# Optimization experiments

Hardware: AMD Instinct MI355X
Metric: run time of the kernel (lower is better)

The kernel has to match this reference:

```python
import jax, jax.numpy as jnp
import numpy as np

B, S, D_IN, D_OUT = 4, 2048, 2048, 2048
E, R = 8, 8
SCALING = 16.0 / 8.0  # lora_alpha / r
# Dropout (p=0.05) treated as identity (eval mode) for a deterministic reference.

def setup_inputs() -> dict:
    key = jax.random.key(0)
    ks = jax.random.split(key, 8)
    x = jax.random.normal(ks[0], (B, S, D_IN), dtype=jnp.float32)
    base_W = jax.random.normal(ks[1], (D_OUT, D_IN), dtype=jnp.float32) * 0.02
    base_b = jax.random.normal(ks[2], (D_OUT,), dtype=jnp.float32) * 0.02
    shared_A = jax.random.normal(ks[3], (R, D_IN), dtype=jnp.float32) * 0.01
    shared_B = jax.random.normal(ks[4], (D_OUT, R), dtype=jnp.float32) * 0.01
    expert_A = jax.random.normal(ks[5], (E, R, D_IN), dtype=jnp.float32) * 0.01
    expert_B = jax.random.normal(ks[6], (E, D_OUT, R), dtype=jnp.float32) * 0.01
    task_emb = jax.random.normal(ks[7], (E, D_IN), dtype=jnp.float32) * 0.01
    collab_w = jnp.array(0.5, dtype=jnp.float32)
    return {"x": x, "base_W": base_W, "base_b": base_b,
            "shared_A": shared_A, "shared_B": shared_B,
            "expert_A": expert_A, "expert_B": expert_B,
            "task_emb": task_emb, "collab_w": collab_w}

def reference(x, base_W, base_b, shared_A, shared_B, expert_A, expert_B, task_emb, collab_w):
    # base linear: [B,S,D_out]
    base_out = jnp.einsum('bsi,oi->bso', x, base_W) + base_b
    # shared LoRA path
    shared_out = jnp.einsum('bsr,or->bso', jnp.einsum('bsi,ri->bsr', x, shared_A), shared_B) * SCALING
    # soft routing over task experts (task_id=None branch)
    x_mean = x.mean(axis=1)                               # [B,D_in]
    routing = jax.nn.softmax(x_mean @ task_emb.T, axis=-1)  # [B,E]
    t = jnp.einsum('bsi,eri->bser', x, expert_A)          # [B,S,E,R] low-rank
    task_out = jnp.einsum('bser,eor,be->bso', t, expert_B, routing) * SCALING
    cw = jax.nn.sigmoid(collab_w)
    return base_out + cw * shared_out + (1.0 - cw) * task_out
```

## Files before the change

kernel.cpp:

```cpp
#include <hip/hip_runtime.h>
#include <hip/hip_bf16.h>
#include <math.h>

#define BATCH 4
#define SEQ   2048
#define DIN   2048
#define DOUT  2048
#define NEXP  8
#define RANK  8
#define MTOT  (BATCH * SEQ)
#define KE    64
#define KAB   96

typedef __bf16 bf16x8 __attribute__((ext_vector_type(8)));
typedef __bf16 bf16x4 __attribute__((ext_vector_type(4)));
typedef float  f32x4  __attribute__((ext_vector_type(4)));

#define GLOBAL_AS __attribute__((address_space(1)))
#define LDS_AS    __attribute__((address_space(3)))

__global__ __launch_bounds__(256) void prep_all(
    const float* __restrict__ x, const float* __restrict__ W,
    const float* __restrict__ expert_A, const float* __restrict__ shared_A,
    const float* __restrict__ expert_B, const float* __restrict__ shared_B,
    const float* __restrict__ task_emb, const float* __restrict__ collab,
    __bf16* __restrict__ xb, __bf16* __restrict__ Wb,
    __bf16* __restrict__ caug, __bf16* __restrict__ Ab)
{
    const int bid = blockIdx.x;
    const int t = threadIdx.x;
    if (bid < 2048) {
        size_t base = (size_t)bid * 8192 + (size_t)t * 32;
        #pragma unroll
        for (int j = 0; j < 4; ++j) {
            float4 v0 = *(const float4*)&x[base + j * 8];
            float4 v1 = *(const float4*)&x[base + j * 8 + 4];
            bf16x8 h = { (__bf16)v0.x, (__bf16)v0.y, (__bf16)v0.z, (__bf16)v0.w,
                         (__bf16)v1.x, (__bf16)v1.y, (__bf16)v1.z, (__bf16)v1.w };
            *(bf16x8*)&xb[base + j * 8] = h;
        }
    } else if (bid < 6144) {
        size_t idx = (size_t)(bid - 2048) * 1024 + t * 4;
        int o = (int)(idx >> 11), i = (int)(idx & 2047);
        float cw = 1.0f / (1.0f + expf(-collab[0]));
        float s = cw * 2.0f;
        float4 w = *(const float4*)&W[idx];
        float dx = 0.f, dy = 0.f, dz = 0.f, dw = 0.f;
        #pragma unroll
        for (int r = 0; r < 8; ++r) {
            float bs = shared_B[(size_t)o * RANK + r];
            float4 as = *(const float4*)&shared_A[(size_t)r * DIN + i];
            dx += bs * as.x; dy += bs * as.y; dz += bs * as.z; dw += bs * as.w;
        }
        bf16x4 h = { (__bf16)(w.x + s * dx), (__bf16)(w.y + s * dy),
                     (__bf16)(w.z + s * dz), (__bf16)(w.w + s * dw) };
        *(bf16x4*)&Wb[idx] = h;
    } else if (bid < 6272) {
        int idx = (bid - 6144) * 1024 + t * 4;
        int o = idx >> 6, k = idx & 63;
        float cw = 1.0f / (1.0f + expf(-collab[0]));
        float s = (1.0f - cw) * 2.0f;
        float4 v = *(const float4*)&expert_B[((size_t)(k >> 3) * DOUT + o) * RANK + (k & 7)];
        bf16x4 h = { (__bf16)(s * v.x), (__bf16)(s * v.y),
                     (__bf16)(s * v.z), (__bf16)(s * v.w) };
        *(bf16x4*)&caug[idx] = h;
    } else {
        int row = bid - 6272;
        int c = t * 8;
        bf16x8 h = { (__bf16)0.f, (__bf16)0.f, (__bf16)0.f, (__bf16)0.f,
                     (__bf16)0.f, (__bf16)0.f, (__bf16)0.f, (__bf16)0.f };
        if (row < 64) {
            float4 v0 = *(const float4*)&expert_A[(size_t)row * DIN + c];
            float4 v1 = *(const float4*)&expert_A[(size_t)row * DIN + c + 4];
            h = bf16x8{ (__bf16)v0.x, (__bf16)v0.y, (__bf16)v0.z, (__bf16)v0.w,
                        (__bf16)v1.x, (__bf16)v1.y, (__bf16)v1.z, (__bf16)v1.w };
        } else if (row < 72) {
            float4 v0 = *(const float4*)&task_emb[(size_t)(row - 64) * DIN + c];
            float4 v1 = *(const float4*)&task_emb[(size_t)(row - 64) * DIN + c + 4];
            h = bf16x8{ (__bf16)v0.x, (__bf16)v0.y, (__bf16)v0.z, (__bf16)v0.w,
                        (__bf16)v1.x, (__bf16)v1.y, (__bf16)v1.z, (__bf16)v1.w };
        }
        *(bf16x8*)&Ab[(size_t)row * DIN + c] = h;
    }
}

__global__ __launch_bounds__(256) void gemm_t(
    const __bf16* __restrict__ xb, const __bf16* __restrict__ Ab,
    __bf16* __restrict__ pt, float* __restrict__ logits)
{
    __shared__ __bf16 lsA[128 * 64];
    __shared__ __bf16 lsB[KAB * 64];
    __shared__ float lsc[32];
    const int bid = blockIdx.x;
    const int t = threadIdx.x;
    const int lane = t & 63;
    const int w = t >> 6;
    const int kc = bid & 3;
    const int m0 = (bid >> 2) * 128;
    const int b  = bid >> 6;

    f32x4 acc[2][5];
    #pragma unroll
    for (int a = 0; a < 2; ++a)
        #pragma unroll
        for (int c = 0; c < 5; ++c) acc[a][c] = (f32x4){0.f, 0.f, 0.f, 0.f};

    for (int k0 = kc * 512; k0 < kc * 512 + 512; k0 += 64) {
        #pragma unroll
        for (int q = 0; q < 4; ++q) {
            int G = q * 256 + t;
            int row = G >> 3, sl = G & 7, seg = sl ^ (row & 7);
            const __bf16* gp = xb + (size_t)(m0 + row) * DIN + k0 + seg * 8;
            __builtin_amdgcn_global_load_lds((GLOBAL_AS void*)gp,
                (LDS_AS void*)&lsA[(q * 256 + (t & ~63)) * 8], 16, 0, 0);
        }
        #pragma unroll
        for (int q = 0; q < 3; ++q) {
            int G = q * 256 + t;
            int row = G >> 3, sl = G & 7, seg = sl ^ (row & 7);
            const __bf16* gp = Ab + (size_t)row * DIN + k0 + seg * 8;
            __builtin_amdgcn_global_load_lds((GLOBAL_AS void*)gp,
                (LDS_AS void*)&lsB[(q * 256 + (t & ~63)) * 8], 16, 0, 0);
        }
        __syncthreads();
        #pragma unroll
        for (int kk = 0; kk < 2; ++kk) {
            bf16x8 af[2], bfr[5];
            #pragma unroll
            for (int tm = 0; tm < 2; ++tm) {
                int r = w * 32 + tm * 16 + (lane & 15);
                int slot = (kk * 4 + (lane >> 4)) ^ (r & 7);
                af[tm] = *(const bf16x8*)&lsA[r * 64 + slot * 8];
            }
            #pragma unroll
            for (int tn = 0; tn < 5; ++tn) {
                int r = tn * 16 + (lane & 15);
                int slot = (kk * 4 + (lane >> 4)) ^ (r & 7);
                bfr[tn] = *(const bf16x8*)&lsB[r * 64 + slot * 8];
            }
            #pragma unroll
            for (int tm = 0; tm < 2; ++tm)
                #pragma unroll
                for (int tn = 0; tn < 5; ++tn)
                    acc[tm][tn] = __builtin_amdgcn_mfma_f32_16x16x32_bf16(
                        af[tm], bfr[tn], acc[tm][tn], 0, 0, 0);
        }
        __syncthreads();
    }

    #pragma unroll
    for (int tm = 0; tm < 2; ++tm)
        #pragma unroll
        for (int tn = 0; tn < 4; ++tn) {
            int col = tn * 16 + (lane & 15);
            #pragma unroll
            for (int v = 0; v < 4; ++v) {
                int row = m0 + w * 32 + tm * 16 + (lane >> 4) * 4 + v;
                pt[((size_t)kc * MTOT + row) * KE + col] = (__bf16)acc[tm][tn][v];
            }
        }

    float s = 0.f;
    #pragma unroll
    for (int tm = 0; tm < 2; ++tm)
        #pragma unroll
        for (int v = 0; v < 4; ++v) s += acc[tm][4][v];
    s += __shfl_down(s, 32);
    s += __shfl_down(s, 16);
    if (lane < 8) lsc[w * 8 + lane] = s;
    __syncthreads();
    if (t < 8) {
        float tot = lsc[t] + lsc[8 + t] + lsc[16 + t] + lsc[24 + t];
        atomicAdd(&logits[b * NEXP + t], tot);
    }
}

__global__ __launch_bounds__(256) void gemm_main(
    const __bf16* __restrict__ xb, const __bf16* __restrict__ Wb,
    const __bf16* __restrict__ pt, const __bf16* __restrict__ caug,
    const float* __restrict__ logits, const float* __restrict__ bias,
    float* __restrict__ out)
{
    __shared__ __bf16 lsA[128 * 64];
    __shared__ __bf16 lsB[128 * 64];
    const int t = threadIdx.x;
    const int lane = t & 63;
    const int wm = (t >> 6) >> 1, wn = (t >> 6) & 1;
    const int m0 = blockIdx.x * 128;
    const int n0 = blockIdx.y * 128;
    const int b  = m0 >> 11;

    float f[NEXP];
    {
        float li[NEXP];
        #pragma unroll
        for (int e = 0; e < NEXP; ++e) li[e] = logits[b * NEXP + e] * (1.0f / (float)SEQ);
        float mx = li[0];
        #pragma unroll
        for (int e = 1; e < NEXP; ++e) mx = fmaxf(mx, li[e]);
        float den = 0.f;
        #pragma unroll
        for (int e = 0; e < NEXP; ++e) { f[e] = expf(li[e] - mx); den += f[e]; }
        float rden = 1.0f / den;
        #pragma unroll
        for (int e = 0; e < NEXP; ++e) f[e] *= rden;
    }

    int rowq[4], segq[4], ldso[4];
    #pragma unroll
    for (int q = 0; q < 4; ++q) {
        rowq[q] = q * 32 + (t >> 3);
        segq[q] = (t & 7) ^ (rowq[q] & 7);
        ldso[q] = (q * 256 + (t & ~63)) * 8;
    }
    int aoff[2][4], boff[2][4];
    #pragma unroll
    for (int tm = 0; tm < 4; ++tm) {
        int r = wm * 64 + tm * 16 + (lane & 15);
        #pragma unroll
        for (int kk = 0; kk < 2; ++kk)
            aoff[kk][tm] = r * 64 + (((kk * 4 + (lane >> 4)) ^ (r & 7)) * 8);
    }
    #pragma unroll
    for (int tn = 0; tn < 4; ++tn) {
        int r = wn * 64 + tn * 16 + (lane & 15);
        #pragma unroll
        for (int kk = 0; kk < 2; ++kk)
            boff[kk][tn] = r * 64 + (((kk * 4 + (lane >> 4)) ^ (r & 7)) * 8);
    }

    f32x4 acc[4][4];
    #pragma unroll
    for (int a = 0; a < 4; ++a)
        #pragma unroll
        for (int c = 0; c < 4; ++c) acc[a][c] = (f32x4){0.f, 0.f, 0.f, 0.f};

    {
        #pragma unroll
        for (int q = 0; q < 4; ++q) {
            const __bf16* gp = caug + (size_t)(n0 + rowq[q]) * KE + segq[q] * 8;
            __builtin_amdgcn_global_load_lds((GLOBAL_AS void*)gp,
                (LDS_AS void*)&lsB[ldso[q]], 16, 0, 0);
        }
        __syncthreads();
        #pragma unroll
        for (int kk = 0; kk < 2; ++kk) {
            float fe = f[kk * 4 + (lane >> 4)];
            bf16x8 afc[4], bfr[4];
            #pragma unroll
            for (int tm = 0; tm < 4; ++tm) {
                int rm = m0 + wm * 64 + tm * 16 + (lane & 15);
                int kb = kk * 32 + (lane >> 4) * 8;
                const __bf16* p0 = pt + (size_t)rm * KE + kb;
                bf16x8 v0 = *(const bf16x8*)(p0);
                bf16x8 v1 = *(const bf16x8*)(p0 + (size_t)MTOT * KE);
                bf16x8 v2 = *(const bf16x8*)(p0 + (size_t)2 * MTOT * KE);
                bf16x8 v3 = *(const bf16x8*)(p0 + (size_t)3 * MTOT * KE);
                bf16x8 r;
                #pragma unroll
                for (int j = 0; j < 8; ++j)
                    r[j] = (__bf16)(((float)v0[j] + (float)v1[j] +
                                     (float)v2[j] + (float)v3[j]) * fe);
                afc[tm] = r;
            }
            #pragma unroll
            for (int tn = 0; tn < 4; ++tn) bfr[tn] = *(const bf16x8*)&lsB[boff[kk][tn]];
            #pragma unroll
            for (int tm = 0; tm < 4; ++tm)
                #pragma unroll
                for (int tn = 0; tn < 4; ++tn)
                    acc[tm][tn] = __builtin_amdgcn_mfma_f32_16x16x32_bf16(
                        afc[tm], bfr[tn], acc[tm][tn], 0, 0, 0);
        }
        __syncthreads();
    }

    const __bf16* pA[4]; const __bf16* pB[4];
    #pragma unroll
    for (int q = 0; q < 4; ++q) {
        pA[q] = xb + (size_t)(m0 + rowq[q]) * DIN + segq[q] * 8;
        pB[q] = Wb + (size_t)(n0 + rowq[q]) * DIN + segq[q] * 8;
    }
    for (int it = 0; it < 32; ++it) {
        #pragma unroll
        for (int q = 0; q < 4; ++q) {
            __builtin_amdgcn_global_load_lds((GLOBAL_AS void*)pA[q],
                (LDS_AS void*)&lsA[ldso[q]], 16, 0, 0);
            __builtin_amdgcn_global_load_lds((GLOBAL_AS void*)pB[q],
                (LDS_AS void*)&lsB[ldso[q]], 16, 0, 0);
            pA[q] += 64; pB[q] += 64;
        }
        __syncthreads();
        #pragma unroll
        for (int kk = 0; kk < 2; ++kk) {
            bf16x8 af[4], bfr[4];
            #pragma unroll
            for (int tm = 0; tm < 4; ++tm) af[tm]  = *(const bf16x8*)&lsA[aoff[kk][tm]];
            #pragma unroll
            for (int tn = 0; tn < 4; ++tn) bfr[tn] = *(const bf16x8*)&lsB[boff[kk][tn]];
            #pragma unroll
            for (int tm = 0; tm < 4; ++tm)
                #pragma unroll
                for (int tn = 0; tn < 4; ++tn)
                    acc[tm][tn] = __builtin_amdgcn_mfma_f32_16x16x32_bf16(
                        af[tm], bfr[tn], acc[tm][tn], 0, 0, 0);
        }
        __syncthreads();
    }

    #pragma unroll
    for (int tm = 0; tm < 4; ++tm)
        #pragma unroll
        for (int tn = 0; tn < 4; ++tn) {
            int col = n0 + wn * 64 + tn * 16 + (lane & 15);
            float bv = bias[col];
            #pragma unroll
            for (int v = 0; v < 4; ++v) {
                int row = m0 + wm * 64 + tm * 16 + (lane >> 4) * 4 + v;
                out[(size_t)row * DOUT + col] = acc[tm][tn][v] + bv;
            }
        }
}

extern "C" void kernel_launch(void* const* d_in, const int* in_sizes, int n_in,
                              void* d_out, int out_size, void* d_ws, size_t ws_size,
                              hipStream_t stream)
{
    const float* x        = (const float*)d_in[0];
    const float* base_W   = (const float*)d_in[1];
    const float* base_b   = (const float*)d_in[2];
    const float* shared_A = (const float*)d_in[3];
    const float* shared_B = (const float*)d_in[4];
    const float* expert_A = (const float*)d_in[5];
    const float* expert_B = (const float*)d_in[6];
    const float* task_emb = (const float*)d_in[7];
    const float* collab_w = (const float*)d_in[8];
    float* out = (float*)d_out;

    char* ws = (char*)d_ws;
    __bf16* xb     = (__bf16*)(ws + 0);
    __bf16* Wb     = (__bf16*)(ws + 33554432);
    __bf16* pt     = (__bf16*)(ws + 41943040);
    __bf16* caug   = (__bf16*)(ws + 46137344);
    __bf16* Ab     = (__bf16*)(ws + 46399488);
    float*  logits = (float*) (ws + 46792704);

    hipMemsetAsync(logits, 0, 256, stream);
    prep_all <<<dim3(6368), 256, 0, stream>>>(x, base_W, expert_A, shared_A,
                                              expert_B, shared_B, task_emb, collab_w,
                                              xb, Wb, caug, Ab);
    gemm_t   <<<dim3(256), 256, 0, stream>>>(xb, Ab, pt, logits);
    gemm_main<<<dim3(64, 16), 256, 0, stream>>>(xb, Wb, pt, caug, logits, base_b, out);
}
```

Before: 257.2 us.

## Precompute routed low-rank activations in separate kernel; move LoRA tile to epilogue

Adds a reduce_route kernel that sums the four split-K partials of the low-rank projection, applies the softmax routing weight, and writes a compact bf16 buffer. gemm_main then loads that buffer through LDS as one extra K=64 step after the main loop, instead of every block reading and reducing the four partials from global memory and recomputing the softmax. prep_all is also re-split into smaller blocks that convert fewer elements per thread. The cost is one extra kernel launch plus a small round trip of the routed buffer through memory.

```diff
diff --git a/kernel.cpp b/kernel.cpp
--- a/kernel.cpp
+++ b/kernel.cpp
@@ -29,18 +29,15 @@
 {
     const int bid = blockIdx.x;
     const int t = threadIdx.x;
-    if (bid < 2048) {
-        size_t base = (size_t)bid * 8192 + (size_t)t * 32;
-        #pragma unroll
-        for (int j = 0; j < 4; ++j) {
-            float4 v0 = *(const float4*)&x[base + j * 8];
-            float4 v1 = *(const float4*)&x[base + j * 8 + 4];
-            bf16x8 h = { (__bf16)v0.x, (__bf16)v0.y, (__bf16)v0.z, (__bf16)v0.w,
-                         (__bf16)v1.x, (__bf16)v1.y, (__bf16)v1.z, (__bf16)v1.w };
-            *(bf16x8*)&xb[base + j * 8] = h;
-        }
-    } else if (bid < 6144) {
-        size_t idx = (size_t)(bid - 2048) * 1024 + t * 4;
+    if (bid < 8192) {
+        size_t base = ((size_t)bid * 256 + t) * 8;
+        float4 v0 = *(const float4*)&x[base];
+        float4 v1 = *(const float4*)&x[base + 4];
+        bf16x8 h = { (__bf16)v0.x, (__bf16)v0.y, (__bf16)v0.z, (__bf16)v0.w,
+                     (__bf16)v1.x, (__bf16)v1.y, (__bf16)v1.z, (__bf16)v1.w };
+        *(bf16x8*)&xb[base] = h;
+    } else if (bid < 12288) {
+        size_t idx = ((size_t)(bid - 8192) * 256 + t) * 4;
         int o = (int)(idx >> 11), i = (int)(idx & 2047);
         float cw = 1.0f / (1.0f + expf(-collab[0]));
         float s = cw * 2.0f;
@@ -55,8 +52,8 @@
         bf16x4 h = { (__bf16)(w.x + s * dx), (__bf16)(w.y + s * dy),
                      (__bf16)(w.z + s * dz), (__bf16)(w.w + s * dw) };
         *(bf16x4*)&Wb[idx] = h;
-    } else if (bid < 6272) {
-        int idx = (bid - 6144) * 1024 + t * 4;
+    } else if (bid < 12416) {
+        int idx = ((bid - 12288) * 256 + t) * 4;
         int o = idx >> 6, k = idx & 63;
         float cw = 1.0f / (1.0f + expf(-collab[0]));
         float s = (1.0f - cw) * 2.0f;
@@ -65,7 +62,7 @@
                      (__bf16)(s * v.z), (__bf16)(s * v.w) };
         *(bf16x4*)&caug[idx] = h;
     } else {
-        int row = bid - 6272;
+        int row = bid - 12416;
         int c = t * 8;
         bf16x8 h = { (__bf16)0.f, (__bf16)0.f, (__bf16)0.f, (__bf16)0.f,
                      (__bf16)0.f, (__bf16)0.f, (__bf16)0.f, (__bf16)0.f };
@@ -175,11 +172,38 @@
     }
 }
 
+__global__ __launch_bounds__(256) void reduce_route(
+    const __bf16* __restrict__ pt, const float* __restrict__ logits,
+    __bf16* __restrict__ tb)
+{
+    size_t idx = ((size_t)blockIdx.x * 256 + threadIdx.x) * 4;
+    int k0 = (int)(idx & 63);
+    int m  = (int)(idx >> 6);
+    int b  = m >> 11;
+    float li[NEXP];
+    #pragma unroll
+    for (int e = 0; e < NEXP; ++e) li[e] = logits[b * NEXP + e] * (1.0f / (float)SEQ);
+    float mx = li[0];
+    #pragma unroll
+    for (int e = 1; e < NEXP; ++e) mx = fmaxf(mx, li[e]);
+    float den = 0.f, ex[NEXP];
+    #pragma unroll
+    for (int e = 0; e < NEXP; ++e) { ex[e] = expf(li[e] - mx); den += ex[e]; }
+    float f = ex[k0 >> 3] / den;
+    float sx = 0.f, sy = 0.f, sz = 0.f, sw = 0.f;
+    #pragma unroll
+    for (int kc = 0; kc < 4; ++kc) {
+        bf16x4 v = *(const bf16x4*)&pt[(size_t)kc * MTOT * KE + idx];
+        sx += (float)v[0]; sy += (float)v[1]; sz += (float)v[2]; sw += (float)v[3];
+    }
+    bf16x4 h = { (__bf16)(sx * f), (__bf16)(sy * f), (__bf16)(sz * f), (__bf16)(sw * f) };
+    *(bf16x4*)&tb[idx] = h;
+}
+
 __global__ __launch_bounds__(256) void gemm_main(
     const __bf16* __restrict__ xb, const __bf16* __restrict__ Wb,
-    const __bf16* __restrict__ pt, const __bf16* __restrict__ caug,
-    const float* __restrict__ logits, const float* __restrict__ bias,
-    float* __restrict__ out)
+    const __bf16* __restrict__ tb, const __bf16* __restrict__ caug,
+    const float* __restrict__ bias, float* __restrict__ out)
 {
     __shared__ __bf16 lsA[128 * 64];
     __shared__ __bf16 lsB[128 * 64];
@@ -188,23 +212,6 @@
     const int wm = (t >> 6) >> 1, wn = (t >> 6) & 1;
     const int m0 = blockIdx.x * 128;
     const int n0 = blockIdx.y * 128;
-    const int b  = m0 >> 11;
-
-    float f[NEXP];
-    {
-        float li[NEXP];
-        #pragma unroll
-        for (int e = 0; e < NEXP; ++e) li[e] = logits[b * NEXP + e] * (1.0f / (float)SEQ);
-        float mx = li[0];
-        #pragma unroll
-        for (int e = 1; e < NEXP; ++e) mx = fmaxf(mx, li[e]);
-        float den = 0.f;
-        #pragma unroll
-        for (int e = 0; e < NEXP; ++e) { f[e] = expf(li[e] - mx); den += f[e]; }
-        float rden = 1.0f / den;
-        #pragma unroll
-        for (int e = 0; e < NEXP; ++e) f[e] *= rden;
-    }
 
     int rowq[4], segq[4], ldso[4];
     #pragma unroll
@@ -213,74 +220,34 @@
         segq[q] = (t & 7) ^ (rowq[q] & 7);
         ldso[q] = (q * 256 + (t & ~63)) * 8;
     }
-    int aoff[2][4], boff[2][4];
-    #pragma unroll
-    for (int tm = 0; tm < 4; ++tm) {
-        int r = wm * 64 + tm * 16 + (lane & 15);
-        #pragma unroll
-        for (int kk = 0; kk < 2; ++kk)
-            aoff[kk][tm] = r * 64 + (((kk * 4 + (lane >> 4)) ^ (r & 7)) * 8);
-    }
-    #pragma unroll
-    for (int tn = 0; tn < 4; ++tn) {
-        int r = wn * 64 + tn * 16 + (lane & 15);
-        #pragma unroll
-        for (int kk = 0; kk < 2; ++kk)
-            boff[kk][tn] = r * 64 + (((kk * 4 + (lane >> 4)) ^ (r & 7)) * 8);
-    }
-
-    f32x4 acc[4][4];
-    #pragma unroll
-    for (int a = 0; a < 4; ++a)
-        #pragma unroll
-        for (int c = 0; c < 4; ++c) acc[a][c] = (f32x4){0.f, 0.f, 0.f, 0.f};
-
-    {
-        #pragma unroll
-        for (int q = 0; q < 4; ++q) {
-            const __bf16* gp = caug + (size_t)(n0 + rowq[q]) * KE + segq[q] * 8;
-            __builtin_amdgcn_global_load_lds((GLOBAL_AS void*)gp,
-                (LDS_AS void*)&lsB[ldso[q]], 16, 0, 0);
-        }
-        __syncthreads();
-        #pragma unroll
-        for (int kk = 0; kk < 2; ++kk) {
-            float fe = f[kk * 4 + (lane >> 4)];
-            bf16x8 afc[4], bfr[4];
-            #pragma unroll
-            for (int tm = 0; tm < 4; ++tm) {
-                int rm = m0 + wm * 64 + tm * 16 + (lane & 15);
-                int kb = kk * 32 + (lane >> 4) * 8;
-                const __bf16* p0 = pt + (size_t)rm * KE + kb;
-                bf16x8 v0 = *(const bf16x8*)(p0);
-                bf16x8 v1 = *(const bf16x8*)(p0 + (size_t)MTOT * KE);
-                bf16x8 v2 = *(const bf16x8*)(p0 + (size_t)2 * MTOT * KE);
-                bf16x8 v3 = *(const bf16x8*)(p0 + (size_t)3 * MTOT * KE);
-                bf16x8 r;
-                #pragma unroll
-                for (int j = 0; j < 8; ++j)
-                    r[j] = (__bf16)(((float)v0[j] + (float)v1[j] +
-                                     (float)v2[j] + (float)v3[j]) * fe);
-                afc[tm] = r;
-            }
-            #pragma unroll
-            for (int tn = 0; tn < 4; ++tn) bfr[tn] = *(const bf16x8*)&lsB[boff[kk][tn]];
-            #pragma unroll
-            for (int tm = 0; tm < 4; ++tm)
-                #pragma unroll
-                for (int tn = 0; tn < 4; ++tn)
-                    acc[tm][tn] = __builtin_amdgcn_mfma_f32_16x16x32_bf16(
-                        afc[tm], bfr[tn], acc[tm][tn], 0, 0, 0);
-        }
-        __syncthreads();
-    }
-
     const __bf16* pA[4]; const __bf16* pB[4];
     #pragma unroll
     for (int q = 0; q < 4; ++q) {
         pA[q] = xb + (size_t)(m0 + rowq[q]) * DIN + segq[q] * 8;
         pB[q] = Wb + (size_t)(n0 + rowq[q]) * DIN + segq[q] * 8;
     }
+    int aoff[2][4], boff[2][4];
+    #pragma unroll
+    for (int tm = 0; tm < 4; ++tm) {
+        int r = wm * 64 + tm * 16 + (lane & 15);
+        #pragma unroll
+        for (int kk = 0; kk < 2; ++kk)
+            aoff[kk][tm] = r * 64 + (((kk * 4 + (lane >> 4)) ^ (r & 7)) * 8);
+    }
+    #pragma unroll
+    for (int tn = 0; tn < 4; ++tn) {
+        int r = wn * 64 + tn * 16 + (lane & 15);
+        #pragma unroll
+        for (int kk = 0; kk < 2; ++kk)
+            boff[kk][tn] = r * 64 + (((kk * 4 + (lane >> 4)) ^ (r & 7)) * 8);
+    }
+
+    f32x4 acc[4][4];
+    #pragma unroll
+    for (int a = 0; a < 4; ++a)
+        #pragma unroll
+        for (int c = 0; c < 4; ++c) acc[a][c] = (f32x4){0.f, 0.f, 0.f, 0.f};
+
     for (int it = 0; it < 32; ++it) {
         #pragma unroll
         for (int q = 0; q < 4; ++q) {
@@ -289,6 +256,34 @@
             __builtin_amdgcn_global_load_lds((GLOBAL_AS void*)pB[q],
                 (LDS_AS void*)&lsB[ldso[q]], 16, 0, 0);
             pA[q] += 64; pB[q] += 64;
+        }
+        __syncthreads();
+        #pragma unroll
+        for (int kk = 0; kk < 2; ++kk) {
+            bf16x8 af[4], bfr[4];
+            #pragma unroll
+            for (int tm = 0; tm < 4; ++tm) af[tm]  = *(const bf16x8*)&lsA[aoff[kk][tm]];
+            #pragma unroll
+            for (int tn = 0; tn < 4; ++tn) bfr[tn] = *(const bf16x8*)&lsB[boff[kk][tn]];
+            #pragma unroll
+            for (int tm = 0; tm < 4; ++tm)
+                #pragma unroll
+                for (int tn = 0; tn < 4; ++tn)
+                    acc[tm][tn] = __builtin_amdgcn_mfma_f32_16x16x32_bf16(
+                        af[tm], bfr[tn], acc[tm][tn], 0, 0, 0);
+        }
+        __syncthreads();
+    }
+
+    {
+        #pragma unroll
+        for (int q = 0; q < 4; ++q) {
+            const __bf16* qA = tb   + (size_t)(m0 + rowq[q]) * KE + segq[q] * 8;
+            const __bf16* qB = caug + (size_t)(n0 + rowq[q]) * KE + segq[q] * 8;
+            __builtin_amdgcn_global_load_lds((GLOBAL_AS void*)qA,
+                (LDS_AS void*)&lsA[ldso[q]], 16, 0, 0);
+            __builtin_amdgcn_global_load_lds((GLOBAL_AS void*)qB,
+                (LDS_AS void*)&lsB[ldso[q]], 16, 0, 0);
         }
         __syncthreads();
         #pragma unroll
@@ -341,14 +336,16 @@
     __bf16* xb     = (__bf16*)(ws + 0);
     __bf16* Wb     = (__bf16*)(ws + 33554432);
     __bf16* pt     = (__bf16*)(ws + 41943040);
-    __bf16* caug   = (__bf16*)(ws + 46137344);
-    __bf16* Ab     = (__bf16*)(ws + 46399488);
-    float*  logits = (float*) (ws + 46792704);
+    __bf16* tb     = (__bf16*)(ws + 46137344);
+    __bf16* caug   = (__bf16*)(ws + 47185920);
+    __bf16* Ab     = (__bf16*)(ws + 47448064);
+    float*  logits = (float*) (ws + 47841280);
 
     hipMemsetAsync(logits, 0, 256, stream);
-    prep_all <<<dim3(6368), 256, 0, stream>>>(x, base_W, expert_A, shared_A,
-                                              expert_B, shared_B, task_emb, collab_w,
-                                              xb, Wb, caug, Ab);
-    gemm_t   <<<dim3(256), 256, 0, stream>>>(xb, Ab, pt, logits);
-    gemm_main<<<dim3(64, 16), 256, 0, stream>>>(xb, Wb, pt, caug, logits, base_b, out);
-}
+    prep_all    <<<dim3(12512), 256, 0, stream>>>(x, base_W, expert_A, shared_A,
+                                                  expert_B, shared_B, task_emb, collab_w,
+                                                  xb, Wb, caug, Ab);
+    gemm_t      <<<dim3(256), 256, 0, stream>>>(xb, Ab, pt, logits);
+    reduce_route<<<dim3(512), 256, 0, stream>>>(pt, logits, tb);
+    gemm_main   <<<dim3(64, 16), 256, 0, stream>>>(xb, Wb, tb, caug, base_b, out);
+}
```

New measurement: 235.4 us. -8.5%, faster.

## Fuse x conversion and low-rank GEMM into prep kernel, move expert pass after main loop

Applied to the files above, without the earlier changes.

The x-to-bf16 conversion, expert_A/task_emb conversion and the low-rank projection GEMM are folded into one prep kernel. Its blocks read fp32 x once, write bf16 xb and use the same tile for the projection with 8 K-chunks, which removes a separate launch and a reread of xb. The atomic logits plus memset are replaced by per-block partial logits that gemm_main reduces itself. The expert correction MFMA pass moves to after the main K loop so the pt and plog reads no longer stall the start of the GEMM. The cost is redundant logit reduction in every gemm_main block and twice as many pt partials to sum.

```diff
diff --git a/kernel.cpp b/kernel.cpp
--- a/kernel.cpp
+++ b/kernel.cpp
@@ -10,7 +10,7 @@
 #define RANK  8
 #define MTOT  (BATCH * SEQ)
 #define KE    64
-#define KAB   96
+#define NKC   8
 
 typedef __bf16 bf16x8 __attribute__((ext_vector_type(8)));
 typedef __bf16 bf16x4 __attribute__((ext_vector_type(4)));
@@ -19,108 +19,92 @@
 #define GLOBAL_AS __attribute__((address_space(1)))
 #define LDS_AS    __attribute__((address_space(3)))
 
-__global__ __launch_bounds__(256) void prep_all(
+__global__ __launch_bounds__(256) void mega_prep(
     const float* __restrict__ x, const float* __restrict__ W,
     const float* __restrict__ expert_A, const float* __restrict__ shared_A,
     const float* __restrict__ expert_B, const float* __restrict__ shared_B,
     const float* __restrict__ task_emb, const float* __restrict__ collab,
     __bf16* __restrict__ xb, __bf16* __restrict__ Wb,
-    __bf16* __restrict__ caug, __bf16* __restrict__ Ab)
+    __bf16* __restrict__ caug, __bf16* __restrict__ pt, float* __restrict__ plog)
 {
     const int bid = blockIdx.x;
     const int t = threadIdx.x;
-    if (bid < 2048) {
-        size_t base = (size_t)bid * 8192 + (size_t)t * 32;
-        #pragma unroll
-        for (int j = 0; j < 4; ++j) {
-            float4 v0 = *(const float4*)&x[base + j * 8];
-            float4 v1 = *(const float4*)&x[base + j * 8 + 4];
+
+    if (bid >= 512) {
+        if (bid < 4608) {
+            size_t idx = ((size_t)(bid - 512) * 256 + t) * 4;
+            int o = (int)(idx >> 11), i = (int)(idx & 2047);
+            float cw = 1.0f / (1.0f + expf(-collab[0]));
+            float s = cw * 2.0f;
+            float4 w = *(const float4*)&W[idx];
+            float dx = 0.f, dy = 0.f, dz = 0.f, dw = 0.f;
+            #pragma unroll
+            for (int r = 0; r < 8; ++r) {
+                float bs = shared_B[(size_t)o * RANK + r];
+                float4 as = *(const float4*)&shared_A[(size_t)r * DIN + i];
+                dx += bs * as.x; dy += bs * as.y; dz += bs * as.z; dw += bs * as.w;
+            }
+            bf16x4 h = { (__bf16)(w.x + s * dx), (__bf16)(w.y + s * dy),
+                         (__bf16)(w.z + s * dz), (__bf16)(w.w + s * dw) };
+            *(bf16x4*)&Wb[idx] = h;
+        } else {
+            int idx = ((bid - 4608) * 256 + t) * 4;
+            int o = idx >> 6, k = idx & 63;
+            float cw = 1.0f / (1.0f + expf(-collab[0]));
+            float s = (1.0f - cw) * 2.0f;
+            float4 v = *(const float4*)&expert_B[((size_t)(k >> 3) * DOUT + o) * RANK + (k & 7)];
+            bf16x4 h = { (__bf16)(s * v.x), (__bf16)(s * v.y),
+                         (__bf16)(s * v.z), (__bf16)(s * v.w) };
+            *(bf16x4*)&caug[idx] = h;
+        }
+        return;
+    }
+
+    __shared__ __bf16 lsA[128 * 64];
+    __shared__ __bf16 lsB[96 * 64];
+    __shared__ float lsc[32];
+    const int lane = t & 63;
+    const int w = t >> 6;
+    const int kc = bid & 7;
+    const int m0 = (bid >> 3) * 128;
+
+    f32x4 acc[2][5];
+    #pragma unroll
+    for (int a = 0; a < 2; ++a)
+        #pragma unroll
+        for (int c = 0; c < 5; ++c) acc[a][c] = (f32x4){0.f, 0.f, 0.f, 0.f};
+
+    for (int it = 0; it < 4; ++it) {
+        int k0 = kc * 256 + it * 64;
+        #pragma unroll
+        for (int q = 0; q < 4; ++q) {
+            int row = q * 32 + (t >> 3), sl = t & 7, seg = sl ^ (row & 7);
+            const float* gp = x + (size_t)(m0 + row) * DIN + k0 + seg * 8;
+            float4 v0 = *(const float4*)gp;
+            float4 v1 = *(const float4*)(gp + 4);
             bf16x8 h = { (__bf16)v0.x, (__bf16)v0.y, (__bf16)v0.z, (__bf16)v0.w,
                          (__bf16)v1.x, (__bf16)v1.y, (__bf16)v1.z, (__bf16)v1.w };
-            *(bf16x8*)&xb[base + j * 8] = h;
-        }
-    } else if (bid < 6144) {
-        size_t idx = (size_t)(bid - 2048) * 1024 + t * 4;
-        int o = (int)(idx >> 11), i = (int)(idx & 2047);
-        float cw = 1.0f / (1.0f + expf(-collab[0]));
-        float s = cw * 2.0f;
-        float4 w = *(const float4*)&W[idx];
-        float dx = 0.f, dy = 0.f, dz = 0.f, dw = 0.f;
-        #pragma unroll
-        for (int r = 0; r < 8; ++r) {
-            float bs = shared_B[(size_t)o * RANK + r];
-            float4 as = *(const float4*)&shared_A[(size_t)r * DIN + i];
-            dx += bs * as.x; dy += bs * as.y; dz += bs * as.z; dw += bs * as.w;
-        }
-        bf16x4 h = { (__bf16)(w.x + s * dx), (__bf16)(w.y + s * dy),
-                     (__bf16)(w.z + s * dz), (__bf16)(w.w + s * dw) };
-        *(bf16x4*)&Wb[idx] = h;
-    } else if (bid < 6272) {
-        int idx = (bid - 6144) * 1024 + t * 4;
-        int o = idx >> 6, k = idx & 63;
-        float cw = 1.0f / (1.0f + expf(-collab[0]));
-        float s = (1.0f - cw) * 2.0f;
-        float4 v = *(const float4*)&expert_B[((size_t)(k >> 3) * DOUT + o) * RANK + (k & 7)];
-        bf16x4 h = { (__bf16)(s * v.x), (__bf16)(s * v.y),
-                     (__bf16)(s * v.z), (__bf16)(s * v.w) };
-        *(bf16x4*)&caug[idx] = h;
-    } else {
-        int row = bid - 6272;
-        int c = t * 8;
-        bf16x8 h = { (__bf16)0.f, (__bf16)0.f, (__bf16)0.f, (__bf16)0.f,
-                     (__bf16)0.f, (__bf16)0.f, (__bf16)0.f, (__bf16)0.f };
-        if (row < 64) {
-            float4 v0 = *(const float4*)&expert_A[(size_t)row * DIN + c];
-            float4 v1 = *(const float4*)&expert_A[(size_t)row * DIN + c + 4];
-            h = bf16x8{ (__bf16)v0.x, (__bf16)v0.y, (__bf16)v0.z, (__bf16)v0.w,
-                        (__bf16)v1.x, (__bf16)v1.y, (__bf16)v1.z, (__bf16)v1.w };
-        } else if (row < 72) {
-            float4 v0 = *(const float4*)&task_emb[(size_t)(row - 64) * DIN + c];
-            float4 v1 = *(const float4*)&task_emb[(size_t)(row - 64) * DIN + c + 4];
-            h = bf16x8{ (__bf16)v0.x, (__bf16)v0.y, (__bf16)v0.z, (__bf16)v0.w,
-                        (__bf16)v1.x, (__bf16)v1.y, (__bf16)v1.z, (__bf16)v1.w };
-        }
-        *(bf16x8*)&Ab[(size_t)row * DIN + c] = h;
-    }
-}
-
-__global__ __launch_bounds__(256) void gemm_t(
-    const __bf16* __restrict__ xb, const __bf16* __restrict__ Ab,
-    __bf16* __restrict__ pt, float* __restrict__ logits)
-{
-    __shared__ __bf16 lsA[128 * 64];
-    __shared__ __bf16 lsB[KAB * 64];
-    __shared__ float lsc[32];
-    const int bid = blockIdx.x;
-    const int t = threadIdx.x;
-    const int lane = t & 63;
-    const int w = t >> 6;
-    const int kc = bid & 3;
-    const int m0 = (bid >> 2) * 128;
-    const int b  = bid >> 6;
-
-    f32x4 acc[2][5];
-    #pragma unroll
-    for (int a = 0; a < 2; ++a)
-        #pragma unroll
-        for (int c = 0; c < 5; ++c) acc[a][c] = (f32x4){0.f, 0.f, 0.f, 0.f};
-
-    for (int k0 = kc * 512; k0 < kc * 512 + 512; k0 += 64) {
-        #pragma unroll
-        for (int q = 0; q < 4; ++q) {
-            int G = q * 256 + t;
-            int row = G >> 3, sl = G & 7, seg = sl ^ (row & 7);
-            const __bf16* gp = xb + (size_t)(m0 + row) * DIN + k0 + seg * 8;
-            __builtin_amdgcn_global_load_lds((GLOBAL_AS void*)gp,
-                (LDS_AS void*)&lsA[(q * 256 + (t & ~63)) * 8], 16, 0, 0);
+            *(bf16x8*)&lsA[row * 64 + sl * 8] = h;
+            *(bf16x8*)&xb[(size_t)(m0 + row) * DIN + k0 + seg * 8] = h;
         }
         #pragma unroll
         for (int q = 0; q < 3; ++q) {
-            int G = q * 256 + t;
-            int row = G >> 3, sl = G & 7, seg = sl ^ (row & 7);
-            const __bf16* gp = Ab + (size_t)row * DIN + k0 + seg * 8;
-            __builtin_amdgcn_global_load_lds((GLOBAL_AS void*)gp,
-                (LDS_AS void*)&lsB[(q * 256 + (t & ~63)) * 8], 16, 0, 0);
+            int c = q * 256 + t;
+            int row = c >> 3, sl = c & 7, seg = sl ^ (row & 7);
+            bf16x8 h = { (__bf16)0.f, (__bf16)0.f, (__bf16)0.f, (__bf16)0.f,
+                         (__bf16)0.f, (__bf16)0.f, (__bf16)0.f, (__bf16)0.f };
+            if (row < 64) {
+                const float* gp = expert_A + (size_t)row * DIN + k0 + seg * 8;
+                float4 v0 = *(const float4*)gp, v1 = *(const float4*)(gp + 4);
+                h = bf16x8{ (__bf16)v0.x, (__bf16)v0.y, (__bf16)v0.z, (__bf16)v0.w,
+                            (__bf16)v1.x, (__bf16)v1.y, (__bf16)v1.z, (__bf16)v1.w };
+            } else if (row < 72) {
+                const float* gp = task_emb + (size_t)(row - 64) * DIN + k0 + seg * 8;
+                float4 v0 = *(const float4*)gp, v1 = *(const float4*)(gp + 4);
+                h = bf16x8{ (__bf16)v0.x, (__bf16)v0.y, (__bf16)v0.z, (__bf16)v0.w,
+                            (__bf16)v1.x, (__bf16)v1.y, (__bf16)v1.z, (__bf16)v1.w };
+            }
+            *(bf16x8*)&lsB[row * 64 + sl * 8] = h;
         }
         __syncthreads();
         #pragma unroll
@@ -169,20 +153,20 @@
     s += __shfl_down(s, 16);
     if (lane < 8) lsc[w * 8 + lane] = s;
     __syncthreads();
-    if (t < 8) {
-        float tot = lsc[t] + lsc[8 + t] + lsc[16 + t] + lsc[24 + t];
-        atomicAdd(&logits[b * NEXP + t], tot);
-    }
+    if (t < 8)
+        plog[bid * 8 + t] = lsc[t] + lsc[8 + t] + lsc[16 + t] + lsc[24 + t];
 }
 
 __global__ __launch_bounds__(256) void gemm_main(
     const __bf16* __restrict__ xb, const __bf16* __restrict__ Wb,
     const __bf16* __restrict__ pt, const __bf16* __restrict__ caug,
-    const float* __restrict__ logits, const float* __restrict__ bias,
+    const float* __restrict__ plog, const float* __restrict__ bias,
     float* __restrict__ out)
 {
     __shared__ __bf16 lsA[128 * 64];
     __shared__ __bf16 lsB[128 * 64];
+    __shared__ float scr[32 * 8];
+    __shared__ float lgs[NEXP];
     const int t = threadIdx.x;
     const int lane = t & 63;
     const int wm = (t >> 6) >> 1, wn = (t >> 6) & 1;
@@ -190,22 +174,6 @@
     const int n0 = blockIdx.y * 128;
     const int b  = m0 >> 11;
 
-    float f[NEXP];
-    {
-        float li[NEXP];
-        #pragma unroll
-        for (int e = 0; e < NEXP; ++e) li[e] = logits[b * NEXP + e] * (1.0f / (float)SEQ);
-        float mx = li[0];
-        #pragma unroll
-        for (int e = 1; e < NEXP; ++e) mx = fmaxf(mx, li[e]);
-        float den = 0.f;
-        #pragma unroll
-        for (int e = 0; e < NEXP; ++e) { f[e] = expf(li[e] - mx); den += f[e]; }
-        float rden = 1.0f / den;
-        #pragma unroll
-        for (int e = 0; e < NEXP; ++e) f[e] *= rden;
-    }
-
     int rowq[4], segq[4], ldso[4];
     #pragma unroll
     for (int q = 0; q < 4; ++q) {
@@ -213,74 +181,34 @@
         segq[q] = (t & 7) ^ (rowq[q] & 7);
         ldso[q] = (q * 256 + (t & ~63)) * 8;
     }
-    int aoff[2][4], boff[2][4];
-    #pragma unroll
-    for (int tm = 0; tm < 4; ++tm) {
-        int r = wm * 64 + tm * 16 + (lane & 15);
-        #pragma unroll
-        for (int kk = 0; kk < 2; ++kk)
-            aoff[kk][tm] = r * 64 + (((kk * 4 + (lane >> 4)) ^ (r & 7)) * 8);
-    }
-    #pragma unroll
-    for (int tn = 0; tn < 4; ++tn) {
-        int r = wn * 64 + tn * 16 + (lane & 15);
-        #pragma unroll
-        for (int kk = 0; kk < 2; ++kk)
-            boff[kk][tn] = r * 64 + (((kk * 4 + (lane >> 4)) ^ (r & 7)) * 8);
-    }
-
-    f32x4 acc[4][4];
-    #pragma unroll
-    for (int a = 0; a < 4; ++a)
-        #pragma unroll
-        for (int c = 0; c < 4; ++c) acc[a][c] = (f32x4){0.f, 0.f, 0.f, 0.f};
-
-    {
-        #pragma unroll
-        for (int q = 0; q < 4; ++q) {
-            const __bf16* gp = caug + (size_t)(n0 + rowq[q]) * KE + segq[q] * 8;
-            __builtin_amdgcn_global_load_lds((GLOBAL_AS void*)gp,
-                (LDS_AS void*)&lsB[ldso[q]], 16, 0, 0);
-        }
-        __syncthreads();
-        #pragma unroll
-        for (int kk = 0; kk < 2; ++kk) {
-            float fe = f[kk * 4 + (lane >> 4)];
-            bf16x8 afc[4], bfr[4];
-            #pragma unroll
-            for (int tm = 0; tm < 4; ++tm) {
-                int rm = m0 + wm * 64 + tm * 16 + (lane & 15);
-                int kb = kk * 32 + (lane >> 4) * 8;
-                const __bf16* p0 = pt + (size_t)rm * KE + kb;
-                bf16x8 v0 = *(const bf16x8*)(p0);
-                bf16x8 v1 = *(const bf16x8*)(p0 + (size_t)MTOT * KE);
-                bf16x8 v2 = *(const bf16x8*)(p0 + (size_t)2 * MTOT * KE);
-                bf16x8 v3 = *(const bf16x8*)(p0 + (size_t)3 * MTOT * KE);
-                bf16x8 r;
-                #pragma unroll
-                for (int j = 0; j < 8; ++j)
-                    r[j] = (__bf16)(((float)v0[j] + (float)v1[j] +
-                                     (float)v2[j] + (float)v3[j]) * fe);
-                afc[tm] = r;
-            }
-            #pragma unroll
-            for (int tn = 0; tn < 4; ++tn) bfr[tn] = *(const bf16x8*)&lsB[boff[kk][tn]];
-            #pragma unroll
-            for (int tm = 0; tm < 4; ++tm)
-                #pragma unroll
-                for (int tn = 0; tn < 4; ++tn)
-                    acc[tm][tn] = __builtin_amdgcn_mfma_f32_16x16x32_bf16(
-                        afc[tm], bfr[tn], acc[tm][tn], 0, 0, 0);
-        }
-        __syncthreads();
-    }
-
     const __bf16* pA[4]; const __bf16* pB[4];
     #pragma unroll
     for (int q = 0; q < 4; ++q) {
         pA[q] = xb + (size_t)(m0 + rowq[q]) * DIN + segq[q] * 8;
         pB[q] = Wb + (size_t)(n0 + rowq[q]) * DIN + segq[q] * 8;
     }
+    int aoff[2][4], boff[2][4];
+    #pragma unroll
+    for (int tm = 0; tm < 4; ++tm) {
+        int r = wm * 64 + tm * 16 + (lane & 15);
+        #pragma unroll
+        for (int kk = 0; kk < 2; ++kk)
+            aoff[kk][tm] = r * 64 + (((kk * 4 + (lane >> 4)) ^ (r & 7)) * 8);
+    }
+    #pragma unroll
+    for (int tn = 0; tn < 4; ++tn) {
+        int r = wn * 64 + tn * 16 + (lane & 15);
+        #pragma unroll
+        for (int kk = 0; kk < 2; ++kk)
+            boff[kk][tn] = r * 64 + (((kk * 4 + (lane >> 4)) ^ (r & 7)) * 8);
+    }
+
+    f32x4 acc[4][4];
+    #pragma unroll
+    for (int a = 0; a < 4; ++a)
+        #pragma unroll
+        for (int c = 0; c < 4; ++c) acc[a][c] = (f32x4){0.f, 0.f, 0.f, 0.f};
+
     for (int it = 0; it < 32; ++it) {
         #pragma unroll
         for (int q = 0; q < 4; ++q) {
@@ -306,6 +234,76 @@
                         af[tm], bfr[tn], acc[tm][tn], 0, 0, 0);
         }
         __syncthreads();
+    }
+
+    #pragma unroll
+    for (int q = 0; q < 4; ++q) {
+        const __bf16* qB = caug + (size_t)(n0 + rowq[q]) * KE + segq[q] * 8;
+        __builtin_amdgcn_global_load_lds((GLOBAL_AS void*)qB,
+            (LDS_AS void*)&lsB[ldso[q]], 16, 0, 0);
+    }
+    {
+        const float* pb = plog + (size_t)b * 128 * 8;
+        int e = t & 7, rr = t >> 3;
+        float part = 0.f;
+        #pragma unroll
+        for (int j = 0; j < 4; ++j) part += pb[(rr + 32 * j) * 8 + e];
+        scr[rr * 8 + e] = part;
+    }
+    __syncthreads();
+    if (t < 8) {
+        float s = 0.f;
+        #pragma unroll
+        for (int i = 0; i < 32; ++i) s += scr[i * 8 + t];
+        lgs[t] = s;
+    }
+    __syncthreads();
+    float f[NEXP];
+    {
+        float li[NEXP];
+        #pragma unroll
+        for (int e = 0; e < NEXP; ++e) li[e] = lgs[e] * (1.0f / (float)SEQ);
+        float mx = li[0];
+        #pragma unroll
+        for (int e = 1; e < NEXP; ++e) mx = fmaxf(mx, li[e]);
+        float den = 0.f;
+        #pragma unroll
+        for (int e = 0; e < NEXP; ++e) { f[e] = expf(li[e] - mx); den += f[e]; }
+        float rden = 1.0f / den;
+        #pragma unroll
+        for (int e = 0; e < NEXP; ++e) f[e] *= rden;
+    }
+    #pragma unroll
+    for (int q = 0; q < 4; ++q) {
+        int row = rowq[q], seg = segq[q];
+        const __bf16* p0 = pt + (size_t)(m0 + row) * KE + seg * 8;
+        float sum[8] = {0.f,0.f,0.f,0.f,0.f,0.f,0.f,0.f};
+        #pragma unroll
+        for (int kc = 0; kc < NKC; ++kc) {
+            bf16x8 v = *(const bf16x8*)(p0 + (size_t)kc * MTOT * KE);
+            #pragma unroll
+            for (int j = 0; j < 8; ++j) sum[j] += (float)v[j];
+        }
+        float fe = f[seg];
+        bf16x8 h;
+        #pragma unroll
+        for (int j = 0; j < 8; ++j) h[j] = (__bf16)(sum[j] * fe);
+        *(bf16x8*)&lsA[row * 64 + (t & 7) * 8] = h;
+    }
+    __syncthreads();
+    #pragma unroll
+    for (int kk = 0; kk < 2; ++kk) {
+        bf16x8 af[4], bfr[4];
+        #pragma unroll
+        for (int tm = 0; tm < 4; ++tm) af[tm]  = *(const bf16x8*)&lsA[aoff[kk][tm]];
+        #pragma unroll
+        for (int tn = 0; tn < 4; ++tn) bfr[tn] = *(const bf16x8*)&lsB[boff[kk][tn]];
+        #pragma unroll
+        for (int tm = 0; tm < 4; ++tm)
+            #pragma unroll
+            for (int tn = 0; tn < 4; ++tn)
+                acc[tm][tn] = __builtin_amdgcn_mfma_f32_16x16x32_bf16(
+                    af[tm], bfr[tn], acc[tm][tn], 0, 0, 0);
     }
 
     #pragma unroll
@@ -338,17 +336,14 @@
     float* out = (float*)d_out;
 
     char* ws = (char*)d_ws;
-    __bf16* xb     = (__bf16*)(ws + 0);
-    __bf16* Wb     = (__bf16*)(ws + 33554432);
-    __bf16* pt     = (__bf16*)(ws + 41943040);
-    __bf16* caug   = (__bf16*)(ws + 46137344);
-    __bf16* Ab     = (__bf16*)(ws + 46399488);
-    float*  logits = (float*) (ws + 46792704);
-
-    hipMemsetAsync(logits, 0, 256, stream);
-    prep_all <<<dim3(6368), 256, 0, stream>>>(x, base_W, expert_A, shared_A,
+    __bf16* xb   = (__bf16*)(ws + 0);
+    __bf16* Wb   = (__bf16*)(ws + 33554432);
+    __bf16* pt   = (__bf16*)(ws + 41943040);
+    __bf16* caug = (__bf16*)(ws + 50331648);
+    float*  plog = (float*) (ws + 50593792);
+
+    mega_prep<<<dim3(4736), 256, 0, stream>>>(x, base_W, expert_A, shared_A,
                                               expert_B, shared_B, task_emb, collab_w,
-                                              xb, Wb, caug, Ab);
-    gemm_t   <<<dim3(256), 256, 0, stream>>>(xb, Ab, pt, logits);
-    gemm_main<<<dim3(64, 16), 256, 0, stream>>>(xb, Wb, pt, caug, logits, base_b, out);
+                                              xb, Wb, caug, pt, plog);
+    gemm_main<<<dim3(64, 16), 256, 0, stream>>>(xb, Wb, pt, caug, plog, base_b, out);
 }
```

Result: faster. 235.2 us (-8.6%).
